# Kernel optimization log

Hardware: AMD Instinct MI355X
Metric: run time of the kernel (lower is better)

Reference implementation:

```python
import jax, jax.numpy as jnp
import numpy as np

GE = 8            # graph_embedding_size
AGG_MEAN = 0.0    # undefined global in source; dataset statistic, fixed here
AGG_VAR = 1.0
N_NODES = 100000
N_EDGES = 3200000


def setup_inputs() -> dict:
    key = jax.random.key(0)
    ks = jax.random.split(key, 17)

    def w(k, shape):
        fan_in = shape[0]
        return jax.random.normal(k, shape, jnp.float32) / np.float32(np.sqrt(fan_in))

    x = jax.random.normal(ks[0], (N_NODES, 1 + GE), jnp.float32)
    edge_attr = jax.random.uniform(ks[1], (N_EDGES, 1), dtype=jnp.float32)
    edge_index = jax.random.randint(ks[2], (2, N_EDGES), 0, N_NODES, dtype=jnp.int32)

    # mlp1: Lin(9,32)+ReLU, Lin(32,32)+ReLU, Lin(32,1)+Sigmoid
    W1, b1 = w(ks[3], (1 + GE, 32)), jnp.zeros((32,), jnp.float32)
    W2, b2 = w(ks[4], (32, 32)), jnp.zeros((32,), jnp.float32)
    W3, b3 = w(ks[5], (32, 1)), jnp.zeros((1,), jnp.float32)
    # mlp2: Lin(10,16)+ReLU, Lin(16,8)+ReLU
    V1, c1 = w(ks[6], (2 + GE, 16)), jnp.zeros((16,), jnp.float32)
    V2, c2 = w(ks[7], (16, GE)), jnp.zeros((GE,), jnp.float32)
    # h2o: Lin(8,16)+ReLU, Lin(16,1)+Sigmoid
    H1, d1 = w(ks[8], (GE, 16)), jnp.zeros((16,), jnp.float32)
    H2, d2 = w(ks[9], (16, 1)), jnp.zeros((1,), jnp.float32)

    return {"x": x, "edge_attr": edge_attr, "edge_index": edge_index,
            "W1": W1, "b1": b1, "W2": W2, "b2": b2, "W3": W3, "b3": b3,
            "V1": V1, "c1": c1, "V2": V2, "c2": c2,
            "H1": H1, "d1": d1, "H2": H2, "d2": d2}


def reference(x, edge_attr, edge_index, W1, b1, W2, b2, W3, b3,
              V1, c1, V2, c2, H1, d1, H2, d2):
    src = edge_index[0]  # x_j gathered from source nodes (PyG default flow)
    dst = edge_index[1]  # aggregate into target nodes
    n = x.shape[0]

    def air_conv(xc):
        xj = xc[src]                                            # [E, 9] gather
        h = jax.nn.relu(xj @ W1 + b1)                           # [E, 32]
        h = jax.nn.relu(h @ W2 + b2)                            # [E, 32]
        msg = jax.nn.sigmoid(h @ W3 + b3) * edge_attr           # [E, 1]
        agg = jax.ops.segment_sum(msg, dst, num_segments=n)     # [N, 1] scatter-add
        norm = (agg - AGG_MEAN) / AGG_VAR
        t = jnp.concatenate([xc, norm], axis=1)                 # [N, 10]
        comb = jax.nn.relu(jax.nn.relu(t @ V1 + c1) @ V2 + c2)  # [N, 8]
        return jnp.concatenate([xc[:, :1], comb], axis=1)       # [N, 9]

    out = air_conv(air_conv(air_conv(x)))
    h = jax.nn.relu(out[:, 1:] @ H1 + d1)                       # [N, 16]
    return jax.nn.sigmoid(h @ H2 + d2)                          # [N, 1]
```

## Files before the change

kernel.cpp:

```cpp
#include <hip/hip_runtime.h>

typedef unsigned int uint;
typedef unsigned short ushort;
typedef unsigned char uchar;


#define NPB 512
#define NPB_SHIFT 9
#define MAXB 256
#define CHUNK 2048
#define S_SPLIT 8
#define NBLK_H 1024

__device__ __forceinline__ void load_smem(float* dstp, const float* __restrict__ srcp,
                                          int n, int tid, int nthreads) {
    for (int i = tid; i < n; i += nthreads) dstp[i] = srcp[i];
}

__device__ __forceinline__ float mlp1_eval(const float* xj,
    const float* sW1, const float* sb1, const float* sW2, const float* sb2,
    const float* sW3, float sb3)
{
    float h1[32];
#pragma unroll
    for (int j = 0; j < 32; ++j) h1[j] = sb1[j];
#pragma unroll
    for (int i = 0; i < 9; ++i) {
        float v = xj[i];
#pragma unroll
        for (int j = 0; j < 32; ++j) h1[j] = fmaf(v, sW1[i*32+j], h1[j]);
    }
#pragma unroll
    for (int j = 0; j < 32; ++j) h1[j] = fmaxf(h1[j], 0.0f);
    float h2[32];
#pragma unroll
    for (int j = 0; j < 32; ++j) h2[j] = sb2[j];
#pragma unroll
    for (int i = 0; i < 32; ++i) {
        float v = h1[i];
#pragma unroll
        for (int j = 0; j < 32; ++j) h2[j] = fmaf(v, sW2[i*32+j], h2[j]);
    }
    float m = sb3;
#pragma unroll
    for (int i = 0; i < 32; ++i) m = fmaf(fmaxf(h2[i], 0.0f), sW3[i], m);
    return 1.0f / (1.0f + __expf(-m));
}

__global__ __launch_bounds__(256) void p0_kernel(
    const float* __restrict__ x,
    const float* __restrict__ W1, const float* __restrict__ b1,
    const float* __restrict__ W2, const float* __restrict__ b2,
    const float* __restrict__ W3, const float* __restrict__ b3,
    float* __restrict__ p, uint* __restrict__ count, float* __restrict__ agg3, int N)
{
    __shared__ float sW1[288], sb1[32], sW2[1024], sb2[32], sW3[32], sb3s[1];
    int tid = threadIdx.x;
    load_smem(sW1, W1, 288, tid, 256);
    load_smem(sb1, b1, 32, tid, 256);
    load_smem(sW2, W2, 1024, tid, 256);
    load_smem(sb2, b2, 32, tid, 256);
    load_smem(sW3, W3, 32, tid, 256);
    if (tid == 0) sb3s[0] = b3[0];
    __syncthreads();
    if (count && blockIdx.x == 0) count[tid] = 0u;
    int n = blockIdx.x * 256 + tid;
    if (n >= N) return;
    if (agg3) { agg3[n] = 0.0f; agg3[N + n] = 0.0f; agg3[2*(size_t)N + n] = 0.0f; }
    float xj[9];
#pragma unroll
    for (int i = 0; i < 9; ++i) xj[i] = x[(size_t)n*9 + i];
    p[n] = mlp1_eval(xj, sW1, sb1, sW2, sb2, sW3, sb3s[0]);
}

__global__ __launch_bounds__(256) void hist_kernel2(
    const int* __restrict__ dst, uint* __restrict__ count, int E, int B)
{
    __shared__ uint hist[MAXB];
    int tid = threadIdx.x;
    for (int i = tid; i < MAXB; i += 256) hist[i] = 0u;
    __syncthreads();
    int total = gridDim.x * 256;
    int gid = blockIdx.x * 256 + tid;
    int E4 = E >> 2;
    const int4* dst4 = (const int4*)dst;
    for (int i = gid; i < E4; i += total) {
        int4 d = dst4[i];
        atomicAdd(&hist[((uint)d.x) >> NPB_SHIFT], 1u);
        atomicAdd(&hist[((uint)d.y) >> NPB_SHIFT], 1u);
        atomicAdd(&hist[((uint)d.z) >> NPB_SHIFT], 1u);
        atomicAdd(&hist[((uint)d.w) >> NPB_SHIFT], 1u);
    }
    for (int e = 4*E4 + gid; e < E; e += total)
        atomicAdd(&hist[((uint)dst[e]) >> NPB_SHIFT], 1u);
    __syncthreads();
    for (int b = tid; b < B; b += 256)
        if (hist[b]) atomicAdd(&count[b], hist[b]);
}

__global__ __launch_bounds__(256) void scan_kernel(
    const uint* __restrict__ count, uint* __restrict__ base,
    uint* __restrict__ cursor, int B)
{
    __shared__ uint s[MAXB];
    int t = threadIdx.x;
    uint v = (t < B) ? count[t] : 0u;
    s[t] = v;
    __syncthreads();
    for (int off = 1; off < MAXB; off <<= 1) {
        uint xv = (t >= off) ? s[t - off] : 0u;
        __syncthreads();
        s[t] += xv;
        __syncthreads();
    }
    uint excl = s[t] - v;
    if (t < B) { base[t] = excl; cursor[t] = excl; }
    else       { cursor[t] = 0u; }
    if (t == B - 1) base[B] = s[t];
}

__global__ __launch_bounds__(256) void partition_kernel(
    const int* __restrict__ dst, const int* __restrict__ src,
    const float* __restrict__ ea, uint* __restrict__ cursor,
    int2* __restrict__ ia, int E, int B)
{
    __shared__ uint hist[MAXB];
    __shared__ uint lbase[MAXB];
    __shared__ uint gbase[MAXB];
    __shared__ int2  payload[CHUNK];
    __shared__ uchar sbin[CHUNK];
    int tid = threadIdx.x;
    int start = blockIdx.x * CHUNK;
    int n = min(E - start, CHUNK);
    hist[tid] = 0u;
    __syncthreads();
    for (int i = tid; i < n; i += 256)
        atomicAdd(&hist[((uint)dst[start + i]) >> NPB_SHIFT], 1u);
    __syncthreads();
    uint cnt_b = hist[tid];
    lbase[tid] = cnt_b;
    __syncthreads();
    for (int o = 1; o < MAXB; o <<= 1) {
        uint xv = (tid >= o) ? lbase[tid - o] : 0u;
        __syncthreads();
        lbase[tid] += xv;
        __syncthreads();
    }
    uint excl = lbase[tid] - cnt_b;
    gbase[tid] = cnt_b ? atomicAdd(&cursor[tid], cnt_b) : 0u;
    lbase[tid] = excl;
    hist[tid]  = excl;
    __syncthreads();
    for (int i = tid; i < n; i += 256) {
        uint d = (uint)dst[start + i];
        uint b = d >> NPB_SHIFT;
        uint s = atomicAdd(&hist[b], 1u);
        int2 v;
        v.x = (int)(((uint)src[start + i] << NPB_SHIFT) | (d & (NPB - 1)));
        v.y = __float_as_int(ea[start + i]);
        payload[s] = v;
        sbin[s] = (uchar)b;
    }
    __syncthreads();
    for (int s2 = tid; s2 < n; s2 += 256) {
        uint b = sbin[s2];
        ia[gbase[b] + ((uint)s2 - lbase[b])] = payload[s2];
    }
}

__global__ __launch_bounds__(512) void agg_kernel(
    const int2* __restrict__ ia, const uint* __restrict__ base,
    const float* __restrict__ p_in, float* __restrict__ aggpart)
{
    __shared__ float aggl[NPB];
    int tid = threadIdx.x;
    int bkt = blockIdx.x / S_SPLIT;
    int sub = blockIdx.x % S_SPLIT;
    aggl[tid] = 0.0f;
    __syncthreads();
    uint e0 = base[bkt], e1 = base[bkt + 1];
    for (uint e = e0 + (uint)sub * 512u + (uint)tid; e < e1; e += S_SPLIT * 512u) {
        int2 v = ia[e];
        atomicAdd(&aggl[(uint)v.x & (NPB - 1)],
                  p_in[(uint)v.x >> NPB_SHIFT] * __int_as_float(v.y));
    }
    __syncthreads();
    aggpart[(size_t)blockIdx.x * NPB + tid] = aggl[tid];
}

template<bool LAST>
__global__ __launch_bounds__(512) void node_kernel2(
    const float* __restrict__ xin, const float* __restrict__ aggpart,
    const float* __restrict__ V1, const float* __restrict__ c1,
    const float* __restrict__ V2, const float* __restrict__ c2,
    const float* __restrict__ W1, const float* __restrict__ b1,
    const float* __restrict__ W2, const float* __restrict__ b2,
    const float* __restrict__ W3, const float* __restrict__ b3,
    const float* __restrict__ H1, const float* __restrict__ d1,
    const float* __restrict__ H2, const float* __restrict__ d2,
    float* __restrict__ xout, float* __restrict__ pout,
    float* __restrict__ finalout, int N)
{
    __shared__ float sV1[160], sc1[16], sV2[128], sc2[8];
    __shared__ float sW1[288], sb1[32], sW2[1024], sb2[32], sW3[32], sbx[1];
    __shared__ float sH1[128], sd1[16], sH2[16], sdx[1];
    int tid = threadIdx.x;
    load_smem(sV1, V1, 160, tid, 512);
    load_smem(sc1, c1, 16, tid, 512);
    load_smem(sV2, V2, 128, tid, 512);
    load_smem(sc2, c2, 8, tid, 512);
    if (!LAST) {
        load_smem(sW1, W1, 288, tid, 512);
        load_smem(sb1, b1, 32, tid, 512);
        load_smem(sW2, W2, 1024, tid, 512);
        load_smem(sb2, b2, 32, tid, 512);
        load_smem(sW3, W3, 32, tid, 512);
        if (tid == 0) sbx[0] = b3[0];
    } else {
        load_smem(sH1, H1, 128, tid, 512);
        load_smem(sd1, d1, 16, tid, 512);
        load_smem(sH2, H2, 16, tid, 512);
        if (tid == 0) sdx[0] = d2[0];
    }
    __syncthreads();

    int bkt = blockIdx.x;
    int n = bkt * NPB + tid;
    if (n >= N) return;

    float aggv = 0.0f;
#pragma unroll
    for (int s = 0; s < S_SPLIT; ++s)
        aggv += aggpart[(size_t)(bkt * S_SPLIT + s) * NPB + tid];

    float t[10];
#pragma unroll
    for (int i = 0; i < 9; ++i) t[i] = xin[(size_t)n*9 + i];
    t[9] = aggv;

    float u[16];
#pragma unroll
    for (int j = 0; j < 16; ++j) u[j] = sc1[j];
#pragma unroll
    for (int i = 0; i < 10; ++i) {
        float v = t[i];
#pragma unroll
        for (int j = 0; j < 16; ++j) u[j] = fmaf(v, sV1[i*16+j], u[j]);
    }
#pragma unroll
    for (int j = 0; j < 16; ++j) u[j] = fmaxf(u[j], 0.0f);

    float comb[8];
#pragma unroll
    for (int j = 0; j < 8; ++j) comb[j] = sc2[j];
#pragma unroll
    for (int i = 0; i < 16; ++i) {
        float v = u[i];
#pragma unroll
        for (int j = 0; j < 8; ++j) comb[j] = fmaf(v, sV2[i*8+j], comb[j]);
    }
#pragma unroll
    for (int j = 0; j < 8; ++j) comb[j] = fmaxf(comb[j], 0.0f);

    if (!LAST) {
        float xnew[9];
        xnew[0] = t[0];
#pragma unroll
        for (int j = 0; j < 8; ++j) xnew[1+j] = comb[j];
#pragma unroll
        for (int i = 0; i < 9; ++i) xout[(size_t)n*9 + i] = xnew[i];
        pout[n] = mlp1_eval(xnew, sW1, sb1, sW2, sb2, sW3, sbx[0]);
    } else {
        float hh[16];
#pragma unroll
        for (int j = 0; j < 16; ++j) hh[j] = sd1[j];
#pragma unroll
        for (int i = 0; i < 8; ++i) {
            float v = comb[i];
#pragma unroll
            for (int j = 0; j < 16; ++j) hh[j] = fmaf(v, sH1[i*16+j], hh[j]);
        }
        float o = sdx[0];
#pragma unroll
        for (int j = 0; j < 16; ++j) o = fmaf(fmaxf(hh[j], 0.0f), sH2[j], o);
        finalout[n] = 1.0f / (1.0f + __expf(-o));
    }
}


__global__ __launch_bounds__(256) void scatter_kernel4(
    const float* __restrict__ p, const int* __restrict__ src, const int* __restrict__ dst,
    const float* __restrict__ eattr, float* __restrict__ agg, int E)
{
    int i = (blockIdx.x * 256 + threadIdx.x) * 4;
    if (i + 3 < E) {
        int4   s = *(const int4*)(src + i);
        int4   d = *(const int4*)(dst + i);
        float4 a = *(const float4*)(eattr + i);
        atomicAdd(&agg[d.x], p[s.x] * a.x);
        atomicAdd(&agg[d.y], p[s.y] * a.y);
        atomicAdd(&agg[d.z], p[s.z] * a.z);
        atomicAdd(&agg[d.w], p[s.w] * a.w);
    } else {
        for (; i < E; ++i) atomicAdd(&agg[dst[i]], p[src[i]] * eattr[i]);
    }
}

template<bool LAST>
__global__ __launch_bounds__(256) void node_kernel(
    const float* __restrict__ xin, const float* __restrict__ agg,
    const float* __restrict__ V1, const float* __restrict__ c1,
    const float* __restrict__ V2, const float* __restrict__ c2,
    const float* __restrict__ W1, const float* __restrict__ b1,
    const float* __restrict__ W2, const float* __restrict__ b2,
    const float* __restrict__ W3, const float* __restrict__ b3,
    const float* __restrict__ H1, const float* __restrict__ d1,
    const float* __restrict__ H2, const float* __restrict__ d2,
    float* __restrict__ xout, float* __restrict__ pout,
    float* __restrict__ finalout, int N)
{
    __shared__ float sV1[160], sc1[16], sV2[128], sc2[8];
    __shared__ float sW1[288], sb1[32], sW2[1024], sb2[32], sW3[32], sbx[1];
    __shared__ float sH1[128], sd1[16], sH2[16], sdx[1];
    int tid = threadIdx.x;
    load_smem(sV1, V1, 160, tid, 256);
    load_smem(sc1, c1, 16, tid, 256);
    load_smem(sV2, V2, 128, tid, 256);
    load_smem(sc2, c2, 8, tid, 256);
    if (!LAST) {
        load_smem(sW1, W1, 288, tid, 256);
        load_smem(sb1, b1, 32, tid, 256);
        load_smem(sW2, W2, 1024, tid, 256);
        load_smem(sb2, b2, 32, tid, 256);
        load_smem(sW3, W3, 32, tid, 256);
        if (tid == 0) sbx[0] = b3[0];
    } else {
        load_smem(sH1, H1, 128, tid, 256);
        load_smem(sd1, d1, 16, tid, 256);
        load_smem(sH2, H2, 16, tid, 256);
        if (tid == 0) sdx[0] = d2[0];
    }
    __syncthreads();
    int n = blockIdx.x * 256 + tid;
    if (n >= N) return;

    float t[10];
#pragma unroll
    for (int i = 0; i < 9; ++i) t[i] = xin[(size_t)n*9 + i];
    t[9] = agg[n];

    float u[16];
#pragma unroll
    for (int j = 0; j < 16; ++j) u[j] = sc1[j];
#pragma unroll
    for (int i = 0; i < 10; ++i) {
        float v = t[i];
#pragma unroll
        for (int j = 0; j < 16; ++j) u[j] = fmaf(v, sV1[i*16+j], u[j]);
    }
#pragma unroll
    for (int j = 0; j < 16; ++j) u[j] = fmaxf(u[j], 0.0f);

    float comb[8];
#pragma unroll
    for (int j = 0; j < 8; ++j) comb[j] = sc2[j];
#pragma unroll
    for (int i = 0; i < 16; ++i) {
        float v = u[i];
#pragma unroll
        for (int j = 0; j < 8; ++j) comb[j] = fmaf(v, sV2[i*8+j], comb[j]);
    }
#pragma unroll
    for (int j = 0; j < 8; ++j) comb[j] = fmaxf(comb[j], 0.0f);

    if (!LAST) {
        float xnew[9];
        xnew[0] = t[0];
#pragma unroll
        for (int j = 0; j < 8; ++j) xnew[1+j] = comb[j];
#pragma unroll
        for (int i = 0; i < 9; ++i) xout[(size_t)n*9 + i] = xnew[i];
        pout[n] = mlp1_eval(xnew, sW1, sb1, sW2, sb2, sW3, sbx[0]);
    } else {
        float hh[16];
#pragma unroll
        for (int j = 0; j < 16; ++j) hh[j] = sd1[j];
#pragma unroll
        for (int i = 0; i < 8; ++i) {
            float v = comb[i];
#pragma unroll
            for (int j = 0; j < 16; ++j) hh[j] = fmaf(v, sH1[i*16+j], hh[j]);
        }
        float o = sdx[0];
#pragma unroll
        for (int j = 0; j < 16; ++j) o = fmaf(fmaxf(hh[j], 0.0f), sH2[j], o);
        finalout[n] = 1.0f / (1.0f + __expf(-o));
    }
}

extern "C" void kernel_launch(void* const* d_in, const int* in_sizes, int n_in,
                              void* d_out, int out_size, void* d_ws, size_t ws_size,
                              hipStream_t stream)
{
    const float* x     = (const float*)d_in[0];
    const float* eattr = (const float*)d_in[1];
    const int*   eidx  = (const int*)d_in[2];
    const float *W1=(const float*)d_in[3],  *b1=(const float*)d_in[4];
    const float *W2=(const float*)d_in[5],  *b2=(const float*)d_in[6];
    const float *W3=(const float*)d_in[7],  *b3=(const float*)d_in[8];
    const float *V1=(const float*)d_in[9],  *c1=(const float*)d_in[10];
    const float *V2=(const float*)d_in[11], *c2=(const float*)d_in[12];
    const float *H1=(const float*)d_in[13], *d1=(const float*)d_in[14];
    const float *H2=(const float*)d_in[15], *d2=(const float*)d_in[16];
    int N = in_sizes[0] / 9;
    int E = in_sizes[1];
    const int* src = eidx;
    const int* dst = eidx + E;
    float* out = (float*)d_out;
    int B = (N + NPB - 1) / NPB;

    size_t need = (size_t)E * 8
                + (size_t)N * 9 * 4
                + (size_t)N * 4 * 2
                + (size_t)B * S_SPLIT * NPB * 4
                + (size_t)MAXB * 4 * 3 + 64;

    dim3 thr256(256), thr512(512);
    dim3 blkN((N + 255) / 256);
    bool packable = ((long long)N << NPB_SHIFT) < (1LL << 32);

    if (B <= MAXB && packable && ws_size >= need) {
        char* w = (char*)d_ws;
        int2*  ia      = (int2*)w;   w += (size_t)E * 8;
        float* xc      = (float*)w;  w += (size_t)N * 9 * 4;
        float* pA      = (float*)w;  w += (size_t)N * 4;
        float* pB      = (float*)w;  w += (size_t)N * 4;
        float* aggpart = (float*)w;  w += (size_t)B * S_SPLIT * NPB * 4;
        uint*  count   = (uint*)w;   w += (size_t)MAXB * 4;
        uint*  cursor  = (uint*)w;   w += (size_t)MAXB * 4;
        uint*  base    = (uint*)w;

        dim3 blkP((E + CHUNK - 1) / CHUNK);
        dim3 blkA(B * S_SPLIT);
        dim3 blkB(B);

        p0_kernel<<<blkN, thr256, 0, stream>>>(x, W1,b1,W2,b2,W3,b3, pA, count, nullptr, N);
        hist_kernel2<<<dim3(NBLK_H), thr256, 0, stream>>>(dst, count, E, B);
        scan_kernel<<<dim3(1), thr256, 0, stream>>>(count, base, cursor, B);
        partition_kernel<<<blkP, thr256, 0, stream>>>(dst, src, eattr, cursor, ia, E, B);

        agg_kernel<<<blkA, thr512, 0, stream>>>(ia, base, pA, aggpart);
        node_kernel2<false><<<blkB, thr512, 0, stream>>>(x, aggpart,
            V1,c1,V2,c2, W1,b1,W2,b2,W3,b3, H1,d1,H2,d2, xc, pB, nullptr, N);
        agg_kernel<<<blkA, thr512, 0, stream>>>(ia, base, pB, aggpart);
        node_kernel2<false><<<blkB, thr512, 0, stream>>>(xc, aggpart,
            V1,c1,V2,c2, W1,b1,W2,b2,W3,b3, H1,d1,H2,d2, xc, pA, nullptr, N);
        agg_kernel<<<blkA, thr512, 0, stream>>>(ia, base, pA, aggpart);
        node_kernel2<true><<<blkB, thr512, 0, stream>>>(xc, aggpart,
            V1,c1,V2,c2, W1,b1,W2,b2,W3,b3, H1,d1,H2,d2, nullptr, nullptr, out, N);
    } else {
        float* ws   = (float*)d_ws;
        float* xcA  = ws;
        float* xcB  = xcA + (size_t)N * 9;
        float* p    = xcB + (size_t)N * 9;
        float* agg3 = p + N;
        dim3 blkE4(((E + 3) / 4 + 255) / 256);

        p0_kernel<<<blkN, thr256, 0, stream>>>(x, W1,b1,W2,b2,W3,b3, p, nullptr, agg3, N);
        scatter_kernel4<<<blkE4, thr256, 0, stream>>>(p, src, dst, eattr, agg3, E);
        node_kernel<false><<<blkN, thr256, 0, stream>>>(x, agg3, V1,c1,V2,c2, W1,b1,W2,b2,W3,b3,
                                                        H1,d1,H2,d2, xcA, p, nullptr, N);
        scatter_kernel4<<<blkE4, thr256, 0, stream>>>(p, src, dst, eattr, agg3 + N, E);
        node_kernel<false><<<blkN, thr256, 0, stream>>>(xcA, agg3 + N, V1,c1,V2,c2, W1,b1,W2,b2,W3,b3,
                                                        H1,d1,H2,d2, xcB, p, nullptr, N);
        scatter_kernel4<<<blkE4, thr256, 0, stream>>>(p, src, dst, eattr, agg3 + 2*(size_t)N, E);
        node_kernel<true><<<blkN, thr256, 0, stream>>>(xcB, agg3 + 2*(size_t)N, V1,c1,V2,c2,
                                                       W1,b1,W2,b2,W3,b3, H1,d1,H2,d2,
                                                       nullptr, nullptr, out, N);
    }
}
```

Measured before the change: 194.2 us.

## Widen destination buckets, streamline partition and vectorize edge aggregation

Buckets grow from 512 to 2048 nodes, so there are about 49 buckets instead of 196. The partition kernel drops its shared-memory staging and local scan: it keeps destinations in registers, builds a small 64-bin histogram, and writes directly to global positions via shared atomics. Bucket sizes are padded to even counts so the aggregation kernel can read two packed edges per 16-byte load with 16-way split blocks. Node kernels now use 256-thread blocks. The risks are scattered, uncoalesced writes in the partition and the partial-sum buffer being read twice as many times per node.

```diff
diff --git a/kernel.cpp b/kernel.cpp
--- a/kernel.cpp
+++ b/kernel.cpp
@@ -1,15 +1,14 @@
 #include <hip/hip_runtime.h>
 
 typedef unsigned int uint;
-typedef unsigned short ushort;
 typedef unsigned char uchar;
 
 
-#define NPB 512
-#define NPB_SHIFT 9
+#define NPB 2048
+#define NPB_SHIFT 11
 #define MAXB 256
-#define CHUNK 2048
-#define S_SPLIT 8
+#define PCHUNK 4096
+#define S_SPLIT 16
 #define NBLK_H 1024
 
 __device__ __forceinline__ void load_smem(float* dstp, const float* __restrict__ srcp,
@@ -104,7 +103,7 @@
 {
     __shared__ uint s[MAXB];
     int t = threadIdx.x;
-    uint v = (t < B) ? count[t] : 0u;
+    uint v = (t < B) ? ((count[t] + 1u) & ~1u) : 0u;
     s[t] = v;
     __syncthreads();
     for (int off = 1; off < MAXB; off <<= 1) {
@@ -119,196 +118,126 @@
     if (t == B - 1) base[B] = s[t];
 }
 
-__global__ __launch_bounds__(256) void partition_kernel(
+__global__ __launch_bounds__(512) void partition_kernel(
     const int* __restrict__ dst, const int* __restrict__ src,
     const float* __restrict__ ea, uint* __restrict__ cursor,
     int2* __restrict__ ia, int E, int B)
 {
-    __shared__ uint hist[MAXB];
-    __shared__ uint lbase[MAXB];
-    __shared__ uint gbase[MAXB];
-    __shared__ int2  payload[CHUNK];
-    __shared__ uchar sbin[CHUNK];
+    __shared__ uint hist[64];
+    __shared__ uint gbase[64];
     int tid = threadIdx.x;
-    int start = blockIdx.x * CHUNK;
-    int n = min(E - start, CHUNK);
-    hist[tid] = 0u;
-    __syncthreads();
-    for (int i = tid; i < n; i += 256)
-        atomicAdd(&hist[((uint)dst[start + i]) >> NPB_SHIFT], 1u);
-    __syncthreads();
-    uint cnt_b = hist[tid];
-    lbase[tid] = cnt_b;
-    __syncthreads();
-    for (int o = 1; o < MAXB; o <<= 1) {
-        uint xv = (tid >= o) ? lbase[tid - o] : 0u;
-        __syncthreads();
-        lbase[tid] += xv;
-        __syncthreads();
-    }
-    uint excl = lbase[tid] - cnt_b;
-    gbase[tid] = cnt_b ? atomicAdd(&cursor[tid], cnt_b) : 0u;
-    lbase[tid] = excl;
-    hist[tid]  = excl;
-    __syncthreads();
-    for (int i = tid; i < n; i += 256) {
-        uint d = (uint)dst[start + i];
-        uint b = d >> NPB_SHIFT;
-        uint s = atomicAdd(&hist[b], 1u);
-        int2 v;
-        v.x = (int)(((uint)src[start + i] << NPB_SHIFT) | (d & (NPB - 1)));
-        v.y = __float_as_int(ea[start + i]);
-        payload[s] = v;
-        sbin[s] = (uchar)b;
-    }
-    __syncthreads();
-    for (int s2 = tid; s2 < n; s2 += 256) {
-        uint b = sbin[s2];
-        ia[gbase[b] + ((uint)s2 - lbase[b])] = payload[s2];
+    int start = blockIdx.x * PCHUNK;
+    int n = min(E - start, PCHUNK);
+    if (tid < 64) hist[tid] = 0u;
+    __syncthreads();
+    uint dc[8];
+#pragma unroll
+    for (int j = 0; j < 2; ++j) {
+        int p4 = tid + j*512;
+        int e  = p4 << 2;
+        if (e + 3 < n) {
+            int4 d = ((const int4*)(dst + start))[p4];
+            dc[j*4+0] = (uint)d.x; dc[j*4+1] = (uint)d.y;
+            dc[j*4+2] = (uint)d.z; dc[j*4+3] = (uint)d.w;
+            atomicAdd(&hist[((uint)d.x) >> NPB_SHIFT], 1u);
+            atomicAdd(&hist[((uint)d.y) >> NPB_SHIFT], 1u);
+            atomicAdd(&hist[((uint)d.z) >> NPB_SHIFT], 1u);
+            atomicAdd(&hist[((uint)d.w) >> NPB_SHIFT], 1u);
+        } else {
+#pragma unroll
+            for (int k = 0; k < 4; ++k) {
+                if (e + k < n) {
+                    uint d = (uint)dst[start + e + k];
+                    dc[j*4+k] = d;
+                    atomicAdd(&hist[d >> NPB_SHIFT], 1u);
+                } else dc[j*4+k] = 0xFFFFFFFFu;
+            }
+        }
+    }
+    __syncthreads();
+    if (tid < 64) {
+        uint c = (tid < B) ? hist[tid] : 0u;
+        gbase[tid] = c ? atomicAdd(&cursor[tid], c) : 0u;
+        hist[tid] = 0u;
+    }
+    __syncthreads();
+#pragma unroll
+    for (int j = 0; j < 2; ++j) {
+        int p4 = tid + j*512;
+        int e  = p4 << 2;
+        if (e + 3 < n) {
+            int4   s4 = ((const int4*)(src + start))[p4];
+            float4 a4 = ((const float4*)(ea + start))[p4];
+            int sv[4] = {s4.x, s4.y, s4.z, s4.w};
+            float av[4] = {a4.x, a4.y, a4.z, a4.w};
+#pragma unroll
+            for (int k = 0; k < 4; ++k) {
+                uint d = dc[j*4+k];
+                uint b = d >> NPB_SHIFT;
+                uint pos = gbase[b] + atomicAdd(&hist[b], 1u);
+                int2 v;
+                v.x = (int)(((uint)sv[k] << NPB_SHIFT) | (d & (NPB - 1)));
+                v.y = __float_as_int(av[k]);
+                ia[pos] = v;
+            }
+        } else {
+#pragma unroll
+            for (int k = 0; k < 4; ++k) {
+                if (e + k < n) {
+                    uint d = dc[j*4+k];
+                    uint b = d >> NPB_SHIFT;
+                    uint pos = gbase[b] + atomicAdd(&hist[b], 1u);
+                    int2 v;
+                    v.x = (int)(((uint)src[start + e + k] << NPB_SHIFT) | (d & (NPB - 1)));
+                    v.y = __float_as_int(ea[start + e + k]);
+                    ia[pos] = v;
+                }
+            }
+        }
     }
 }
 
 __global__ __launch_bounds__(512) void agg_kernel(
     const int2* __restrict__ ia, const uint* __restrict__ base,
-    const float* __restrict__ p_in, float* __restrict__ aggpart)
+    const uint* __restrict__ count, const float* __restrict__ p_in,
+    float* __restrict__ aggpart)
 {
     __shared__ float aggl[NPB];
     int tid = threadIdx.x;
     int bkt = blockIdx.x / S_SPLIT;
     int sub = blockIdx.x % S_SPLIT;
-    aggl[tid] = 0.0f;
-    __syncthreads();
-    uint e0 = base[bkt], e1 = base[bkt + 1];
-    for (uint e = e0 + (uint)sub * 512u + (uint)tid; e < e1; e += S_SPLIT * 512u) {
-        int2 v = ia[e];
-        atomicAdd(&aggl[(uint)v.x & (NPB - 1)],
-                  p_in[(uint)v.x >> NPB_SHIFT] * __int_as_float(v.y));
-    }
-    __syncthreads();
-    aggpart[(size_t)blockIdx.x * NPB + tid] = aggl[tid];
+#pragma unroll
+    for (int k = 0; k < NPB/512; ++k) aggl[tid + k*512] = 0.0f;
+    __syncthreads();
+    uint e0 = base[bkt];
+    uint e1 = e0 + count[bkt];
+    for (uint estart = e0 + (uint)sub * 4096u; estart < e1;
+         estart += (uint)S_SPLIT * 4096u) {
+#pragma unroll
+        for (int j = 0; j < 4; ++j) {
+            uint e = estart + 2u * ((uint)tid + (uint)j * 512u);
+            if (e + 1u < e1) {
+                int4 w = *(const int4*)(ia + e);
+                float m0 = p_in[(uint)w.x >> NPB_SHIFT] * __int_as_float(w.y);
+                float m1 = p_in[(uint)w.z >> NPB_SHIFT] * __int_as_float(w.w);
+                atomicAdd(&aggl[(uint)w.x & (NPB - 1)], m0);
+                atomicAdd(&aggl[(uint)w.z & (NPB - 1)], m1);
+            } else if (e < e1) {
+                int2 w = ia[e];
+                atomicAdd(&aggl[(uint)w.x & (NPB - 1)],
+                          p_in[(uint)w.x >> NPB_SHIFT] * __int_as_float(w.y));
+            }
+        }
+    }
+    __syncthreads();
+#pragma unroll
+    for (int k = 0; k < NPB/512; ++k)
+        aggpart[(size_t)blockIdx.x * NPB + tid + k*512] = aggl[tid + k*512];
 }
 
 template<bool LAST>
-__global__ __launch_bounds__(512) void node_kernel2(
+__global__ __launch_bounds__(256) void node_kernel3(
     const float* __restrict__ xin, const float* __restrict__ aggpart,
-    const float* __restrict__ V1, const float* __restrict__ c1,
-    const float* __restrict__ V2, const float* __restrict__ c2,
-    const float* __restrict__ W1, const float* __restrict__ b1,
-    const float* __restrict__ W2, const float* __restrict__ b2,
-    const float* __restrict__ W3, const float* __restrict__ b3,
-    const float* __restrict__ H1, const float* __restrict__ d1,
-    const float* __restrict__ H2, const float* __restrict__ d2,
-    float* __restrict__ xout, float* __restrict__ pout,
-    float* __restrict__ finalout, int N)
-{
-    __shared__ float sV1[160], sc1[16], sV2[128], sc2[8];
-    __shared__ float sW1[288], sb1[32], sW2[1024], sb2[32], sW3[32], sbx[1];
-    __shared__ float sH1[128], sd1[16], sH2[16], sdx[1];
-    int tid = threadIdx.x;
-    load_smem(sV1, V1, 160, tid, 512);
-    load_smem(sc1, c1, 16, tid, 512);
-    load_smem(sV2, V2, 128, tid, 512);
-    load_smem(sc2, c2, 8, tid, 512);
-    if (!LAST) {
-        load_smem(sW1, W1, 288, tid, 512);
-        load_smem(sb1, b1, 32, tid, 512);
-        load_smem(sW2, W2, 1024, tid, 512);
-        load_smem(sb2, b2, 32, tid, 512);
-        load_smem(sW3, W3, 32, tid, 512);
-        if (tid == 0) sbx[0] = b3[0];
-    } else {
-        load_smem(sH1, H1, 128, tid, 512);
-        load_smem(sd1, d1, 16, tid, 512);
-        load_smem(sH2, H2, 16, tid, 512);
-        if (tid == 0) sdx[0] = d2[0];
-    }
-    __syncthreads();
-
-    int bkt = blockIdx.x;
-    int n = bkt * NPB + tid;
-    if (n >= N) return;
-
-    float aggv = 0.0f;
-#pragma unroll
-    for (int s = 0; s < S_SPLIT; ++s)
-        aggv += aggpart[(size_t)(bkt * S_SPLIT + s) * NPB + tid];
-
-    float t[10];
-#pragma unroll
-    for (int i = 0; i < 9; ++i) t[i] = xin[(size_t)n*9 + i];
-    t[9] = aggv;
-
-    float u[16];
-#pragma unroll
-    for (int j = 0; j < 16; ++j) u[j] = sc1[j];
-#pragma unroll
-    for (int i = 0; i < 10; ++i) {
-        float v = t[i];
-#pragma unroll
-        for (int j = 0; j < 16; ++j) u[j] = fmaf(v, sV1[i*16+j], u[j]);
-    }
-#pragma unroll
-    for (int j = 0; j < 16; ++j) u[j] = fmaxf(u[j], 0.0f);
-
-    float comb[8];
-#pragma unroll
-    for (int j = 0; j < 8; ++j) comb[j] = sc2[j];
-#pragma unroll
-    for (int i = 0; i < 16; ++i) {
-        float v = u[i];
-#pragma unroll
-        for (int j = 0; j < 8; ++j) comb[j] = fmaf(v, sV2[i*8+j], comb[j]);
-    }
-#pragma unroll
-    for (int j = 0; j < 8; ++j) comb[j] = fmaxf(comb[j], 0.0f);
-
-    if (!LAST) {
-        float xnew[9];
-        xnew[0] = t[0];
-#pragma unroll
-        for (int j = 0; j < 8; ++j) xnew[1+j] = comb[j];
-#pragma unroll
-        for (int i = 0; i < 9; ++i) xout[(size_t)n*9 + i] = xnew[i];
-        pout[n] = mlp1_eval(xnew, sW1, sb1, sW2, sb2, sW3, sbx[0]);
-    } else {
-        float hh[16];
-#pragma unroll
-        for (int j = 0; j < 16; ++j) hh[j] = sd1[j];
-#pragma unroll
-        for (int i = 0; i < 8; ++i) {
-            float v = comb[i];
-#pragma unroll
-            for (int j = 0; j < 16; ++j) hh[j] = fmaf(v, sH1[i*16+j], hh[j]);
-        }
-        float o = sdx[0];
-#pragma unroll
-        for (int j = 0; j < 16; ++j) o = fmaf(fmaxf(hh[j], 0.0f), sH2[j], o);
-        finalout[n] = 1.0f / (1.0f + __expf(-o));
-    }
-}
-
-
-__global__ __launch_bounds__(256) void scatter_kernel4(
-    const float* __restrict__ p, const int* __restrict__ src, const int* __restrict__ dst,
-    const float* __restrict__ eattr, float* __restrict__ agg, int E)
-{
-    int i = (blockIdx.x * 256 + threadIdx.x) * 4;
-    if (i + 3 < E) {
-        int4   s = *(const int4*)(src + i);
-        int4   d = *(const int4*)(dst + i);
-        float4 a = *(const float4*)(eattr + i);
-        atomicAdd(&agg[d.x], p[s.x] * a.x);
-        atomicAdd(&agg[d.y], p[s.y] * a.y);
-        atomicAdd(&agg[d.z], p[s.z] * a.z);
-        atomicAdd(&agg[d.w], p[s.w] * a.w);
-    } else {
-        for (; i < E; ++i) atomicAdd(&agg[dst[i]], p[src[i]] * eattr[i]);
-    }
-}
-
-template<bool LAST>
-__global__ __launch_bounds__(256) void node_kernel(
-    const float* __restrict__ xin, const float* __restrict__ agg,
     const float* __restrict__ V1, const float* __restrict__ c1,
     const float* __restrict__ V2, const float* __restrict__ c2,
     const float* __restrict__ W1, const float* __restrict__ b1,
@@ -341,6 +270,124 @@
         if (tid == 0) sdx[0] = d2[0];
     }
     __syncthreads();
+
+    int n = blockIdx.x * 256 + tid;
+    if (n >= N) return;
+
+    int bkt = n >> NPB_SHIFT, slot = n & (NPB - 1);
+    const float* ap = aggpart + (size_t)bkt * S_SPLIT * NPB + slot;
+    float aggv = 0.0f;
+#pragma unroll
+    for (int s = 0; s < S_SPLIT; ++s) aggv += ap[(size_t)s * NPB];
+
+    float t[10];
+#pragma unroll
+    for (int i = 0; i < 9; ++i) t[i] = xin[(size_t)n*9 + i];
+    t[9] = aggv;
+
+    float u[16];
+#pragma unroll
+    for (int j = 0; j < 16; ++j) u[j] = sc1[j];
+#pragma unroll
+    for (int i = 0; i < 10; ++i) {
+        float v = t[i];
+#pragma unroll
+        for (int j = 0; j < 16; ++j) u[j] = fmaf(v, sV1[i*16+j], u[j]);
+    }
+#pragma unroll
+    for (int j = 0; j < 16; ++j) u[j] = fmaxf(u[j], 0.0f);
+
+    float comb[8];
+#pragma unroll
+    for (int j = 0; j < 8; ++j) comb[j] = sc2[j];
+#pragma unroll
+    for (int i = 0; i < 16; ++i) {
+        float v = u[i];
+#pragma unroll
+        for (int j = 0; j < 8; ++j) comb[j] = fmaf(v, sV2[i*8+j], comb[j]);
+    }
+#pragma unroll
+    for (int j = 0; j < 8; ++j) comb[j] = fmaxf(comb[j], 0.0f);
+
+    if (!LAST) {
+        float xnew[9];
+        xnew[0] = t[0];
+#pragma unroll
+        for (int j = 0; j < 8; ++j) xnew[1+j] = comb[j];
+#pragma unroll
+        for (int i = 0; i < 9; ++i) xout[(size_t)n*9 + i] = xnew[i];
+        pout[n] = mlp1_eval(xnew, sW1, sb1, sW2, sb2, sW3, sbx[0]);
+    } else {
+        float hh[16];
+#pragma unroll
+        for (int j = 0; j < 16; ++j) hh[j] = sd1[j];
+#pragma unroll
+        for (int i = 0; i < 8; ++i) {
+            float v = comb[i];
+#pragma unroll
+            for (int j = 0; j < 16; ++j) hh[j] = fmaf(v, sH1[i*16+j], hh[j]);
+        }
+        float o = sdx[0];
+#pragma unroll
+        for (int j = 0; j < 16; ++j) o = fmaf(fmaxf(hh[j], 0.0f), sH2[j], o);
+        finalout[n] = 1.0f / (1.0f + __expf(-o));
+    }
+}
+
+
+__global__ __launch_bounds__(256) void scatter_kernel4(
+    const float* __restrict__ p, const int* __restrict__ src, const int* __restrict__ dst,
+    const float* __restrict__ eattr, float* __restrict__ agg, int E)
+{
+    int i = (blockIdx.x * 256 + threadIdx.x) * 4;
+    if (i + 3 < E) {
+        int4   s = *(const int4*)(src + i);
+        int4   d = *(const int4*)(dst + i);
+        float4 a = *(const float4*)(eattr + i);
+        atomicAdd(&agg[d.x], p[s.x] * a.x);
+        atomicAdd(&agg[d.y], p[s.y] * a.y);
+        atomicAdd(&agg[d.z], p[s.z] * a.z);
+        atomicAdd(&agg[d.w], p[s.w] * a.w);
+    } else {
+        for (; i < E; ++i) atomicAdd(&agg[dst[i]], p[src[i]] * eattr[i]);
+    }
+}
+
+template<bool LAST>
+__global__ __launch_bounds__(256) void node_kernel(
+    const float* __restrict__ xin, const float* __restrict__ agg,
+    const float* __restrict__ V1, const float* __restrict__ c1,
+    const float* __restrict__ V2, const float* __restrict__ c2,
+    const float* __restrict__ W1, const float* __restrict__ b1,
+    const float* __restrict__ W2, const float* __restrict__ b2,
+    const float* __restrict__ W3, const float* __restrict__ b3,
+    const float* __restrict__ H1, const float* __restrict__ d1,
+    const float* __restrict__ H2, const float* __restrict__ d2,
+    float* __restrict__ xout, float* __restrict__ pout,
+    float* __restrict__ finalout, int N)
+{
+    __shared__ float sV1[160], sc1[16], sV2[128], sc2[8];
+    __shared__ float sW1[288], sb1[32], sW2[1024], sb2[32], sW3[32], sbx[1];
+    __shared__ float sH1[128], sd1[16], sH2[16], sdx[1];
+    int tid = threadIdx.x;
+    load_smem(sV1, V1, 160, tid, 256);
+    load_smem(sc1, c1, 16, tid, 256);
+    load_smem(sV2, V2, 128, tid, 256);
+    load_smem(sc2, c2, 8, tid, 256);
+    if (!LAST) {
+        load_smem(sW1, W1, 288, tid, 256);
+        load_smem(sb1, b1, 32, tid, 256);
+        load_smem(sW2, W2, 1024, tid, 256);
+        load_smem(sb2, b2, 32, tid, 256);
+        load_smem(sW3, W3, 32, tid, 256);
+        if (tid == 0) sbx[0] = b3[0];
+    } else {
+        load_smem(sH1, H1, 128, tid, 256);
+        load_smem(sd1, d1, 16, tid, 256);
+        load_smem(sH2, H2, 16, tid, 256);
+        if (tid == 0) sdx[0] = d2[0];
+    }
+    __syncthreads();
     int n = blockIdx.x * 256 + tid;
     if (n >= N) return;
 
@@ -419,7 +466,7 @@
     float* out = (float*)d_out;
     int B = (N + NPB - 1) / NPB;
 
-    size_t need = (size_t)E * 8
+    size_t need = (size_t)(E + MAXB) * 8
                 + (size_t)N * 9 * 4
                 + (size_t)N * 4 * 2
                 + (size_t)B * S_SPLIT * NPB * 4
@@ -431,7 +478,7 @@
 
     if (B <= MAXB && packable && ws_size >= need) {
         char* w = (char*)d_ws;
-        int2*  ia      = (int2*)w;   w += (size_t)E * 8;
+        int2*  ia      = (int2*)w;   w += (size_t)(E + MAXB) * 8;
         float* xc      = (float*)w;  w += (size_t)N * 9 * 4;
         float* pA      = (float*)w;  w += (size_t)N * 4;
         float* pB      = (float*)w;  w += (size_t)N * 4;
@@ -440,23 +487,22 @@
         uint*  cursor  = (uint*)w;   w += (size_t)MAXB * 4;
         uint*  base    = (uint*)w;
 
-        dim3 blkP((E + CHUNK - 1) / CHUNK);
+        dim3 blkP((E + PCHUNK - 1) / PCHUNK);
         dim3 blkA(B * S_SPLIT);
-        dim3 blkB(B);
 
         p0_kernel<<<blkN, thr256, 0, stream>>>(x, W1,b1,W2,b2,W3,b3, pA, count, nullptr, N);
         hist_kernel2<<<dim3(NBLK_H), thr256, 0, stream>>>(dst, count, E, B);
         scan_kernel<<<dim3(1), thr256, 0, stream>>>(count, base, cursor, B);
-        partition_kernel<<<blkP, thr256, 0, stream>>>(dst, src, eattr, cursor, ia, E, B);
-
-        agg_kernel<<<blkA, thr512, 0, stream>>>(ia, base, pA, aggpart);
-        node_kernel2<false><<<blkB, thr512, 0, stream>>>(x, aggpart,
+        partition_kernel<<<blkP, thr512, 0, stream>>>(dst, src, eattr, cursor, ia, E, B);
+
+        agg_kernel<<<blkA, thr512, 0, stream>>>(ia, base, count, pA, aggpart);
+        node_kernel3<false><<<blkN, thr256, 0, stream>>>(x, aggpart,
             V1,c1,V2,c2, W1,b1,W2,b2,W3,b3, H1,d1,H2,d2, xc, pB, nullptr, N);
-        agg_kernel<<<blkA, thr512, 0, stream>>>(ia, base, pB, aggpart);
-        node_kernel2<false><<<blkB, thr512, 0, stream>>>(xc, aggpart,
+        agg_kernel<<<blkA, thr512, 0, stream>>>(ia, base, count, pB, aggpart);
+        node_kernel3<false><<<blkN, thr256, 0, stream>>>(xc, aggpart,
             V1,c1,V2,c2, W1,b1,W2,b2,W3,b3, H1,d1,H2,d2, xc, pA, nullptr, N);
-        agg_kernel<<<blkA, thr512, 0, stream>>>(ia, base, pA, aggpart);
-        node_kernel2<true><<<blkB, thr512, 0, stream>>>(xc, aggpart,
+        agg_kernel<<<blkA, thr512, 0, stream>>>(ia, base, count, pA, aggpart);
+        node_kernel3<true><<<blkN, thr256, 0, stream>>>(xc, aggpart,
             V1,c1,V2,c2, W1,b1,W2,b2,W3,b3, H1,d1,H2,d2, nullptr, nullptr, out, N);
     } else {
         float* ws   = (float*)d_ws;
```

New measurement: 171.9 us. 11.5% less time.
